# Kernel tuning notes

Hardware: AMD Instinct MI355X
Metric: run time of the kernel (lower is better)

Reference implementation:

```python
import jax, jax.numpy as jnp
import numpy as np

L, B, D = 2048, 16, 1024
SCALE_X = (1.0 + 2.0 * float(np.exp(0.0))) ** 0.5  # rescale=True, highway_bias=0 -> sqrt(3)


def setup_inputs() -> dict:
    key = jax.random.key(0)
    k1, k2, k3 = jax.random.split(key, 3)
    x = jax.random.normal(k1, (L, B, D), dtype=jnp.float32)
    c0 = jnp.zeros((B, D), dtype=jnp.float32)
    # Xavier-ish scale (3/d)^0.5 as in reset_parameters
    val_range = (3.0 / D) ** 0.5
    weight = jax.random.uniform(k2, (D, 3 * D), dtype=jnp.float32,
                                minval=-val_range, maxval=val_range)
    weight_c = jax.random.uniform(k3, (2 * D,), dtype=jnp.float32,
                                  minval=-val_range, maxval=val_range)
    bias = jnp.zeros((2 * D,), dtype=jnp.float32)
    return {"x": x, "c0": c0, "weight": weight, "weight_c": weight_c, "bias": bias}


def _sru_forward(x, c0, weight, weight_c, bias):
    # u = x @ W, viewed as [L, B, D, 3] (k = 3)
    u = jnp.einsum('lbi,io->lbo', x, weight).reshape(L, B, D, 3)
    fw, rw = weight_c[:D], weight_c[D:]      # per-feature recurrent gate weights
    fb, rb = bias[:D], bias[D:]              # forget / reset biases
    u0 = u[..., 0]                           # [L, B, D] candidate
    u1 = u[..., 1] + fb                      # forget pre-activation
    u2 = u[..., 2] + rb                      # reset pre-activation
    xp = x * SCALE_X                         # highway term (k==3, skip via x)

    def step(c_prev, inputs):
        u0_t, u1_t, u2_t, xp_t = inputs
        f = jax.nn.sigmoid(u1_t + c_prev * fw)
        r = jax.nn.sigmoid(u2_t + c_prev * rw)
        c = u0_t + (c_prev - u0_t) * f
        g = c  # activation_type == 0 (identity)
        h = xp_t + (g - xp_t) * r
        return c, h

    c_final, h = jax.lax.scan(step, c0, (u0, u1, u2, xp))
    return h, c_final


def reference(x, c0, weight, weight_c, bias):
    return _sru_forward(x, c0, weight, weight_c, bias)
```

## Files before the change

kernel.cpp:

```cpp
#include <hip/hip_runtime.h>
#include <stdint.h>

#define L_DIM 2048
#define B_DIM 16
#define D_DIM 1024
#define M_DIM 32768
#define K_DIM 1024
#define N_DIM 3072
#define SCALE_X 1.7320508075688772f

typedef __attribute__((ext_vector_type(8))) short short8;
typedef __attribute__((ext_vector_type(8))) unsigned short ushort8;
typedef __attribute__((ext_vector_type(4))) float f32x4;

__device__ __forceinline__ float bf2f(uint32_t b) {
    union { uint32_t u; float f; } v; v.u = b << 16; return v.f;
}
__device__ __forceinline__ uint16_t f2bf(float f) {
    union { float f; uint32_t u; } v; v.f = f;
    uint32_t u = v.u;
    return (uint16_t)((u + 0x7FFFu + ((u >> 16) & 1u)) >> 16);
}

__device__ __forceinline__ void gl16(const uint16_t* g, uint16_t* l) {
    __builtin_amdgcn_global_load_lds(
        (const __attribute__((address_space(1))) void*)g,
        (__attribute__((address_space(3))) void*)l,
        16 , 0, 0);
}

__device__ __forceinline__ void fence_all() {
    asm volatile("" ::: "memory");
    __builtin_amdgcn_sched_barrier(0);
}
__device__ __forceinline__ void barrier_hard() {
    fence_all();
    __builtin_amdgcn_s_barrier();
    fence_all();
}

__global__ void prep_w_kernel(const float* __restrict__ w, uint16_t* __restrict__ wt) {
    int i = blockIdx.x * 256 + threadIdx.x;
    int k = i / N_DIM;
    int n = i - k * N_DIM;
    wt[n * K_DIM + k] = f2bf(w[i]);
}

__global__ void __launch_bounds__(256)
prep_x_kernel(const float* __restrict__ x, uint16_t* __restrict__ xb) {
    size_t i = (size_t)blockIdx.x * 256 + threadIdx.x;
    const float4 a = *(const float4*)(x + i * 8);
    const float4 b = *(const float4*)(x + i * 8 + 4);
    ushort8 o;
    o[0] = f2bf(a.x); o[1] = f2bf(a.y); o[2] = f2bf(a.z); o[3] = f2bf(a.w);
    o[4] = f2bf(b.x); o[5] = f2bf(b.y); o[6] = f2bf(b.z); o[7] = f2bf(b.w);
    *(ushort8*)(xb + i * 8) = o;
}

__global__ void __launch_bounds__(512, 2)
gemm_8ph_kernel(const uint16_t* __restrict__ Ab,
                const uint16_t* __restrict__ Bt,
                uint16_t* __restrict__ u01,
                uint16_t* __restrict__ u2p)
{
    __shared__ uint16_t lds[65536];

    int bid = blockIdx.x;
    int mg = bid / 96;
    int tt = bid - mg * 96;
    int ntile = tt >> 3;
    int mtile = mg * 8 + (tt & 7);
    int m0 = mtile * 256;
    int n0 = ntile * 256;

    int t = threadIdx.x;
    int lane = t & 63;
    int w = t >> 6;
    int wm = (w >> 2) * 128;
    int wn = (w & 3) * 64;

    int row0 = t >> 3;
    int slot = t & 7;
    int swz_c = (slot ^ (row0 & 7)) * 8;
    const uint16_t* pA = Ab + (((size_t)(m0 + row0)) << 10) + swz_c;
    const uint16_t* pB = Bt + (((size_t)(n0 + row0)) << 10) + swz_c;

    int frow = lane & 15;
    int fkb = (lane >> 4) * 16;

    f32x4 acc[8][4] = {};
    short8 aF[4][2];
    short8 bF[4][2];

#define STAGE(hh, Tn) { \
    const uint16_t* gs = (((hh) < 2) ? pA : pB) + ((size_t)((hh) & 1) * 131072) + (size_t)(Tn) * 64; \
    uint16_t* ld = lds + nxtO + (hh) * 8192 + t * 8; \
    gl16(gs, ld); gl16(gs + 65536, ld + 4096); }

#define RD_A(mh) { \
    _Pragma("unroll") for (int mf = 0; mf < 4; mf++) \
    _Pragma("unroll") for (int ks = 0; ks < 2; ks++) { \
        int r = wm + (mh) * 64 + mf * 16 + frow; \
        int cb = (ks * 64 + fkb) ^ ((r & 7) << 4); \
        aF[mf][ks] = *(const short8*)(lds + curA + r * 64 + (cb >> 1)); } }

#define RD_B() { \
    _Pragma("unroll") for (int nf = 0; nf < 4; nf++) \
    _Pragma("unroll") for (int ks = 0; ks < 2; ks++) { \
        int r = wn + nf * 16 + frow; \
        int cb = (ks * 64 + fkb) ^ ((r & 7) << 4); \
        bF[nf][ks] = *(const short8*)(lds + curB + r * 64 + (cb >> 1)); } }

#define QM(mh, nh) { \
    __builtin_amdgcn_s_setprio(1); \
    _Pragma("unroll") for (int mf = 0; mf < 4; mf++) \
    _Pragma("unroll") for (int nj = 0; nj < 2; nj++) \
    _Pragma("unroll") for (int ks = 0; ks < 2; ks++) \
        acc[(mh) * 4 + mf][(nh) * 2 + nj] = __builtin_amdgcn_mfma_f32_16x16x32_bf16( \
            aF[mf][ks], bF[(nh) * 2 + nj][ks], acc[(mh) * 4 + mf][(nh) * 2 + nj], 0, 0, 0); \
    __builtin_amdgcn_s_setprio(0); }

    {
        int nxtO = 0;
        STAGE(0, 0); STAGE(1, 0); STAGE(2, 0); STAGE(3, 0);
    }

    for (int T = 0; T < 15; ++T) {
        int cur = T & 1;
        int curA = cur * 32768;
        int curB = curA + 16384;
        int nxtO = (cur ^ 1) * 32768;

        barrier_hard();
        STAGE(0, T + 1);
        fence_all();
        asm volatile("s_waitcnt vmcnt(2)" ::: "memory");
        barrier_hard();
        RD_B();
        RD_A(0);
        QM(0, 0);
        fence_all();
        STAGE(1, T + 1);
        fence_all();
        QM(0, 1);
        RD_A(1);
        fence_all();
        STAGE(2, T + 1);
        fence_all();
        QM(1, 1);
        fence_all();
        STAGE(3, T + 1);
        fence_all();
        QM(1, 0);
    }

    {
        int curA = 32768;
        int curB = curA + 16384;
        barrier_hard();
        asm volatile("s_waitcnt vmcnt(0)" ::: "memory");
        barrier_hard();
        RD_B();
        RD_A(0);
        QM(0, 0);
        QM(0, 1);
        RD_A(1);
        QM(1, 1);
        QM(1, 0);
    }

#undef STAGE
#undef RD_A
#undef RD_B
#undef QM

    int colf = lane & 15;
    int rowq = (lane >> 4) * 4;
#pragma unroll
    for (int i = 0; i < 8; i++) {
#pragma unroll
        for (int j = 0; j < 4; j++) {
            int gcol = n0 + wn + j * 16 + colf;
            int dq = gcol / 3;
            int cm = gcol - dq * 3;
#pragma unroll
            for (int r = 0; r < 4; r++) {
                int grow = m0 + wm + i * 16 + rowq + r;
                uint16_t v = f2bf(acc[i][j][r]);
                if (cm < 2) u01[(size_t)grow * 2048 + dq * 2 + cm] = v;
                else        u2p[(size_t)grow * 1024 + dq] = v;
            }
        }
    }
}

__global__ void __launch_bounds__(256)
gemm_kernel(const float* __restrict__ A32,
            const uint16_t* __restrict__ Bt,
            uint16_t* __restrict__ u01,
            uint16_t* __restrict__ u2p)
{
    __shared__ uint16_t As[128 * 32];
    __shared__ uint16_t Bs[128 * 32];

    int bid = blockIdx.x;
    int mg = bid / 192;
    int tt = bid - mg * 192;
    int ntile = tt >> 3;
    int mtile = mg * 8 + (tt & 7);
    int m0 = mtile * 128;
    int n0 = ntile * 128;

    int t = threadIdx.x;
    int lane = t & 63;
    int w = t >> 6;
    int wm = (w >> 1) * 64;
    int wn = (w & 1) * 64;

    f32x4 acc[4][4] = {};

    int frow = lane & 15;
    int fk = (lane >> 4) * 8;

    for (int kt = 0; kt < K_DIM; kt += 32) {
#pragma unroll
        for (int c = 0; c < 4; c++) {
            int idx = c * 256 + t;
            int row = idx >> 3;
            int ko = (idx & 7) * 4;
            float4 v = *(const float4*)(A32 + (size_t)(m0 + row) * K_DIM + kt + ko);
            ushort4 o;
            o.x = f2bf(v.x); o.y = f2bf(v.y); o.z = f2bf(v.z); o.w = f2bf(v.w);
            *(ushort4*)(As + row * 32 + ko) = o;
        }
#pragma unroll
        for (int c = 0; c < 2; c++) {
            int idx = c * 256 + t;
            int row = idx >> 2;
            int ko = (idx & 3) * 8;
            short8 v = *(const short8*)(Bt + (size_t)(n0 + row) * K_DIM + kt + ko);
            *(short8*)(Bs + row * 32 + ko) = v;
        }
        __syncthreads();

        short8 af[4], bfr[4];
#pragma unroll
        for (int i = 0; i < 4; i++) {
            af[i]  = *(const short8*)(As + (wm + i * 16 + frow) * 32 + fk);
            bfr[i] = *(const short8*)(Bs + (wn + i * 16 + frow) * 32 + fk);
        }
#pragma unroll
        for (int i = 0; i < 4; i++)
#pragma unroll
            for (int j = 0; j < 4; j++)
                acc[i][j] = __builtin_amdgcn_mfma_f32_16x16x32_bf16(af[i], bfr[j], acc[i][j], 0, 0, 0);
        __syncthreads();
    }

    int colf = lane & 15;
    int rowq = (lane >> 4) * 4;
#pragma unroll
    for (int i = 0; i < 4; i++) {
#pragma unroll
        for (int j = 0; j < 4; j++) {
            int gcol = n0 + wn + j * 16 + colf;
            int dq = gcol / 3;
            int cm = gcol - dq * 3;
#pragma unroll
            for (int r = 0; r < 4; r++) {
                int grow = m0 + wm + i * 16 + rowq + r;
                uint16_t v = f2bf(acc[i][j][r]);
                if (cm < 2) u01[(size_t)grow * 2048 + dq * 2 + cm] = v;
                else        u2p[(size_t)grow * 1024 + dq] = v;
            }
        }
    }
}

__global__ void __launch_bounds__(64)
scan_kernel(const uint32_t* u01,
            const uint16_t* __restrict__ u2p,
            const float* __restrict__ x,
            const float* __restrict__ c0,
            const float* __restrict__ wc,
            const float* __restrict__ bias,
            float* out)
{
    int cid = blockIdx.x * 64 + threadIdx.x;
    int d = cid & (D_DIM - 1);
    float fw = wc[d], rw = wc[D_DIM + d];
    float fb = bias[d], rb = bias[D_DIM + d];
    float c = c0[cid];

    constexpr int P = 16;
    const int STEP = B_DIM * D_DIM;
    uint32_t b01[P];
    uint16_t b2v[P];
    float bx[P];
#pragma unroll
    for (int j = 0; j < P; j++) {
        b01[j] = u01[cid + j * STEP];
        b2v[j] = u2p[cid + j * STEP];
        bx[j]  = x[cid + j * STEP];
    }

    for (int lb = 0; lb < L_DIM; lb += P) {
#pragma unroll
        for (int j = 0; j < P; j++) {
            int l = lb + j;
            uint32_t v01 = b01[j];
            float u2 = bf2f((uint32_t)b2v[j]);
            float xp = bx[j] * SCALE_X;

            int ln = l + P; if (ln > L_DIM - 1) ln = L_DIM - 1;
            int ri = cid + ln * STEP;
            b01[j] = u01[ri];
            b2v[j] = u2p[ri];
            bx[j]  = x[ri];

            float u0 = bf2f(v01 & 0xFFFFu);
            float u1 = bf2f(v01 >> 16);

            float ef = __expf(-(u1 + fb + c * fw));
            float er = __expf(-(u2 + rb + c * rw));
            float f = __builtin_amdgcn_rcpf(1.0f + ef);
            float r = __builtin_amdgcn_rcpf(1.0f + er);
            c = u0 + (c - u0) * f;
            float h = xp + (c - xp) * r;
            out[l * STEP + cid] = h;
        }
    }
    out[L_DIM * STEP + cid] = c;
}

extern "C" void kernel_launch(void* const* d_in, const int* in_sizes, int n_in,
                              void* d_out, int out_size, void* d_ws, size_t ws_size,
                              hipStream_t stream) {
    const float* x    = (const float*)d_in[0];
    const float* c0   = (const float*)d_in[1];
    const float* w    = (const float*)d_in[2];
    const float* wc   = (const float*)d_in[3];
    const float* bias = (const float*)d_in[4];

    uint16_t* wt  = (uint16_t*)d_ws;
    uint16_t* u2p = (uint16_t*)((char*)d_ws + 6291456);
    const size_t XB_OFF = 6291456 + (size_t)M_DIM * D_DIM * 2;
    const size_t WS_NEED = XB_OFF + (size_t)M_DIM * K_DIM * 2;

    uint16_t* u01 = (uint16_t*)d_out;
    float* out = (float*)d_out;

    prep_w_kernel<<<(K_DIM * N_DIM) / 256, 256, 0, stream>>>(w, wt);

    if (ws_size >= WS_NEED) {
        uint16_t* xb = (uint16_t*)((char*)d_ws + XB_OFF);
        prep_x_kernel<<<(M_DIM * K_DIM / 8) / 256, 256, 0, stream>>>(x, xb);
        gemm_8ph_kernel<<<(M_DIM / 256) * (N_DIM / 256), 512, 0, stream>>>(xb, wt, u01, u2p);
    } else {
        gemm_kernel<<<(M_DIM / 128) * (N_DIM / 128), 256, 0, stream>>>(x, wt, u01, u2p);
    }

    scan_kernel<<<(B_DIM * D_DIM) / 64, 64, 0, stream>>>((const uint32_t*)u01, u2p, x,
                                                         c0, wc, bias, out);
}
```

Before: 690.6 us.

## Split scan into serial c recurrence and parallel h pass; tile weight transpose

```diff
diff --git a/kernel.cpp b/kernel.cpp
--- a/kernel.cpp
+++ b/kernel.cpp
@@ -39,11 +39,21 @@
     fence_all();
 }
 
-__global__ void prep_w_kernel(const float* __restrict__ w, uint16_t* __restrict__ wt) {
-    int i = blockIdx.x * 256 + threadIdx.x;
-    int k = i / N_DIM;
-    int n = i - k * N_DIM;
-    wt[n * K_DIM + k] = f2bf(w[i]);
+__global__ void __launch_bounds__(256)
+prep_w_kernel(const float* __restrict__ w, uint16_t* __restrict__ wt) {
+    __shared__ uint16_t tile[32][33];
+    int bid = blockIdx.x;
+    int kt = (bid & 31) * 32;
+    int nt = (bid >> 5) * 32;
+    int tx = threadIdx.x & 31;
+    int ty = threadIdx.x >> 5;
+#pragma unroll
+    for (int r = 0; r < 32; r += 8)
+        tile[ty + r][tx] = f2bf(w[(size_t)(kt + ty + r) * N_DIM + nt + tx]);
+    __syncthreads();
+#pragma unroll
+    for (int r = 0; r < 32; r += 8)
+        wt[(size_t)(nt + ty + r) * K_DIM + kt + tx] = tile[tx][ty + r];
 }
 
 __global__ void __launch_bounds__(256)
@@ -278,13 +288,12 @@
 }
 
 __global__ void __launch_bounds__(64)
-scan_kernel(const uint32_t* u01,
-            const uint16_t* __restrict__ u2p,
-            const float* __restrict__ x,
-            const float* __restrict__ c0,
-            const float* __restrict__ wc,
-            const float* __restrict__ bias,
-            float* out)
+scan_c_kernel(const uint32_t* u01,
+              uint16_t* u2io,
+              const float* __restrict__ c0,
+              const float* __restrict__ wc,
+              const float* __restrict__ bias,
+              float* out)
 {
     int cid = blockIdx.x * 64 + threadIdx.x;
     int d = cid & (D_DIM - 1);
@@ -295,13 +304,11 @@
     constexpr int P = 16;
     const int STEP = B_DIM * D_DIM;
     uint32_t b01[P];
-    uint16_t b2v[P];
-    float bx[P];
+    uint16_t b2[P];
 #pragma unroll
     for (int j = 0; j < P; j++) {
         b01[j] = u01[cid + j * STEP];
-        b2v[j] = u2p[cid + j * STEP];
-        bx[j]  = x[cid + j * STEP];
+        b2[j]  = u2io[cid + j * STEP];
     }
 
     for (int lb = 0; lb < L_DIM; lb += P) {
@@ -309,28 +316,47 @@
         for (int j = 0; j < P; j++) {
             int l = lb + j;
             uint32_t v01 = b01[j];
-            float u2 = bf2f((uint32_t)b2v[j]);
-            float xp = bx[j] * SCALE_X;
+            float u2 = bf2f((uint32_t)b2[j]);
 
             int ln = l + P; if (ln > L_DIM - 1) ln = L_DIM - 1;
-            int ri = cid + ln * STEP;
-            b01[j] = u01[ri];
-            b2v[j] = u2p[ri];
-            bx[j]  = x[ri];
+            b01[j] = u01[cid + ln * STEP];
+            b2[j]  = u2io[cid + ln * STEP];
 
             float u0 = bf2f(v01 & 0xFFFFu);
             float u1 = bf2f(v01 >> 16);
-
-            float ef = __expf(-(u1 + fb + c * fw));
-            float er = __expf(-(u2 + rb + c * rw));
+            float cp = c;
+            float ef = __expf(-(u1 + fb + cp * fw));
             float f = __builtin_amdgcn_rcpf(1.0f + ef);
-            float r = __builtin_amdgcn_rcpf(1.0f + er);
-            c = u0 + (c - u0) * f;
-            float h = xp + (c - xp) * r;
-            out[l * STEP + cid] = h;
+            c = u0 + (cp - u0) * f;
+            float rarg = u2 + rb + cp * rw;
+            out[l * STEP + cid] = c;
+            u2io[l * STEP + cid] = f2bf(rarg);
         }
     }
     out[L_DIM * STEP + cid] = c;
+}
+
+__global__ void __launch_bounds__(256)
+h_kernel(float* out,
+         const uint16_t* __restrict__ rargp,
+         const float* __restrict__ x)
+{
+    size_t i = ((size_t)blockIdx.x * 256 + threadIdx.x) * 4;
+
+    f32x4 cv = *(const f32x4*)(out + i);
+    f32x4 xv = *(const f32x4*)(x + i);
+    ushort4 uv = *(const ushort4*)(rargp + i);
+
+    float ra[4] = { bf2f(uv.x), bf2f(uv.y), bf2f(uv.z), bf2f(uv.w) };
+    f32x4 h;
+#pragma unroll
+    for (int e = 0; e < 4; e++) {
+        float xp = xv[e] * SCALE_X;
+        float er = __expf(-ra[e]);
+        float r = __builtin_amdgcn_rcpf(1.0f + er);
+        h[e] = xp + (cv[e] - xp) * r;
+    }
+    *(f32x4*)(out + i) = h;
 }
 
 extern "C" void kernel_launch(void* const* d_in, const int* in_sizes, int n_in,
@@ -350,7 +376,7 @@
     uint16_t* u01 = (uint16_t*)d_out;
     float* out = (float*)d_out;
 
-    prep_w_kernel<<<(K_DIM * N_DIM) / 256, 256, 0, stream>>>(w, wt);
+    prep_w_kernel<<<(K_DIM / 32) * (N_DIM / 32), 256, 0, stream>>>(w, wt);
 
     if (ws_size >= WS_NEED) {
         uint16_t* xb = (uint16_t*)((char*)d_ws + XB_OFF);
@@ -360,6 +386,7 @@
         gemm_kernel<<<(M_DIM / 128) * (N_DIM / 128), 256, 0, stream>>>(x, wt, u01, u2p);
     }
 
-    scan_kernel<<<(B_DIM * D_DIM) / 64, 64, 0, stream>>>((const uint32_t*)u01, u2p, x,
-                                                         c0, wc, bias, out);
-}
+    scan_c_kernel<<<(B_DIM * D_DIM) / 64, 64, 0, stream>>>((const uint32_t*)u01, u2p,
+                                                           c0, wc, bias, out);
+    h_kernel<<<(M_DIM * D_DIM / 4) / 256, 256, 0, stream>>>(out, u2p, x);
+}
```

After: 699.4 us. Within noise of the previous version (+1.3%).
